# Optimization experiments

Hardware: AMD Instinct MI355X
Metric: run time of the kernel (lower is better)

The kernel has to match this reference:

```python
import jax, jax.numpy as jnp
import numpy as np

B, L, D = 8, 2048, 256
D_MODEL = 1024
NUM_SIGNALS = 16
MAX_POSITIONS = 4096
ROLE_OUTPUT = 2  # role id used for the CLS token


def setup_inputs() -> dict:
    key = jax.random.key(0)
    ks = jax.random.split(key, 12)
    emb = jax.random.normal(ks[0], (B, L, D), dtype=jnp.float32)
    pos = jax.random.randint(ks[1], (B, L), 1, MAX_POSITIONS + 1)          # pos >= 1 for real tokens
    sid = jax.random.randint(ks[2], (B, L), 0, NUM_SIGNALS)
    role = jax.random.randint(ks[3], (B, L), 0, 3)
    padding_mask = jax.random.uniform(ks[4], (B, L)) < 0.75                # True = real token
    # learned parameters
    proj_W = jax.random.normal(ks[5], (NUM_SIGNALS, D_MODEL, D), dtype=jnp.float32) * (1.0 / np.sqrt(D))
    proj_b = jax.random.normal(ks[6], (NUM_SIGNALS, D_MODEL), dtype=jnp.float32) * 0.01
    cls_content = jax.random.normal(ks[7], (D_MODEL,), dtype=jnp.float32)
    pos_embed = jax.random.normal(ks[8], (MAX_POSITIONS + 1, D_MODEL), dtype=jnp.float32)
    id_embed = jax.random.normal(ks[9], (NUM_SIGNALS + 1, D_MODEL), dtype=jnp.float32)
    role_embed = jax.random.normal(ks[10], (3, D_MODEL), dtype=jnp.float32)
    return dict(emb=emb, pos=pos, sid=sid, role=role, padding_mask=padding_mask,
                proj_W=proj_W, proj_b=proj_b, cls_content=cls_content,
                pos_embed=pos_embed, id_embed=id_embed, role_embed=role_embed)


def reference(emb, pos, sid, role, padding_mask,
              proj_W, proj_b, cls_content, pos_embed, id_embed, role_embed):
    Bv, Lv, _ = emb.shape
    S, d_model, _ = proj_W.shape
    cls_id = S

    # Grouped per-signal projection: one GEMM per signal id, select per token.
    tokens = jnp.zeros((Bv, Lv, d_model), dtype=emb.dtype)
    for s in range(S):
        proj_s = jnp.einsum('bld,ed->ble', emb, proj_W[s]) + proj_b[s]   # (B, L, d_model)
        keep = ((sid == s) & padding_mask)[..., None]
        tokens = jnp.where(keep, proj_s, tokens)

    # Prepend CLS
    cls = jnp.broadcast_to(cls_content[None, None, :], (Bv, 1, d_model))
    tokens = jnp.concatenate([cls, tokens], axis=1)                       # (B, L+1, d_model)

    pos_full = jnp.concatenate([jnp.zeros((Bv, 1), dtype=pos.dtype), pos], axis=1)
    sid_full = jnp.concatenate([jnp.full((Bv, 1), cls_id, dtype=sid.dtype), sid], axis=1)
    role_full = jnp.concatenate([jnp.full((Bv, 1), ROLE_OUTPUT, dtype=role.dtype), role], axis=1)

    tokens = tokens + pos_embed[pos_full] + id_embed[sid_full] + role_embed[role_full]

    attn_keep = jnp.concatenate([jnp.ones((Bv, 1), dtype=bool), padding_mask], axis=1)
    return tokens, attn_keep
```

## Files before the change

kernel.cpp:

```cpp
#include <hip/hip_runtime.h>
#include <hip/hip_bf16.h>
#include <stdint.h>

#define B_ 8
#define L_ 2048
#define NTOK 16384
#define DK 256
#define DM 1024
#define NS 16
#define LOUT 2049
#define TOK_OUT (B_*LOUT*DM)
#define ATTN_OUT (B_*LOUT)
#define PCAP 2048
#define UCAP 8192

typedef unsigned short u16;
typedef unsigned int u32;
typedef __bf16 bf16x8 __attribute__((ext_vector_type(8)));
typedef float f32x4 __attribute__((ext_vector_type(4)));

__device__ inline u32 packbf2(float lo, float hi) {
    u32 a, b;
    __builtin_memcpy(&a, &lo, 4);
    __builtin_memcpy(&b, &hi, 4);
    a = (a + 0x8000u) >> 16;
    b = (b + 0x8000u) & 0xFFFF0000u;
    return a | b;
}

__device__ inline void gll16(const void* g, void* l) {
    __builtin_amdgcn_global_load_lds(
        (const __attribute__((address_space(1))) unsigned int*)g,
        (__attribute__((address_space(3))) unsigned int*)l, 16, 0, 0);
}

#define WS_CUR 0
#define WS_UCUR 16
#define WS_WIDTH 32
#define WS_PERM 64
#define WS_UNM (64 + NS * PCAP)
#define EMB_OFF 262144ULL
#define W_OFF (EMB_OFF + 16384ULL * 512ULL)
#define WS_NEED (W_OFF + 16384ULL * 512ULL)

__device__ inline int sniff_width(const unsigned char* mb, int tid, int* sh) {
    if (tid == 0) { sh[0] = 0; sh[1] = 0; sh[2] = 0; }
    __syncthreads();
    int c1ge2 = 0, ge2 = 0, oddnz = 0;
    const u32* mw = (const u32*)mb;
    #pragma unroll
    for (int i = 0; i < 16; i++) {
        u32 x = mw[tid * 16 + i];
        u32 b0 = x & 0xFF, b1 = (x >> 8) & 0xFF, b2 = (x >> 16) & 0xFF, b3 = x >> 24;
        if (b1 >= 2) c1ge2 = 1;
        if (b0 >= 2 || b1 >= 2 || b2 >= 2 || b3 >= 2) ge2 = 1;
        if ((b1 | b3) != 0) oddnz = 1;
    }
    if (c1ge2) atomicOr(&sh[0], 1);
    if (ge2) atomicOr(&sh[1], 1);
    if (oddnz) atomicOr(&sh[2], 1);
    __syncthreads();
    if (sh[0]) return 2;
    if (sh[1]) return 4;
    if (sh[2]) return 1;
    return 4;
}

__device__ inline int decode_mask(const unsigned char* mb, int t, int width) {
    if (width == 1) return mb[t] != 0;
    if (width == 2) return ((const u16*)mb)[t] != 0;
    return ((const u32*)mb)[t] != 0;
}

#define SORT_B 64
#define PREP_GRID (SORT_B + 1024)

__global__ __launch_bounds__(256) void prep_all(
    const unsigned char* __restrict__ mb, const int* __restrict__ sid,
    const float* __restrict__ emb, const float* __restrict__ W,
    int* __restrict__ wsi, unsigned char* __restrict__ wsb) {
    __shared__ int sh[3];
    __shared__ int lcnt[NS], gbase[NS];
    __shared__ int lcnt_u, gbase_u;
    int bid = blockIdx.x;
    int tid = threadIdx.x;
    int lane = tid & 63;
    int wv = tid >> 6;

    if (bid < SORT_B) {
        if (tid < NS) lcnt[tid] = 0;
        if (tid == 0) lcnt_u = 0;
        int width = sniff_width(mb, tid, sh);
        if (bid == 0 && tid == 0) wsi[WS_WIDTH] = width;
        int t = bid * 256 + tid;
        int m = decode_mask(mb, t, width);
        int s = sid[t];
        int lr;
        if (m) lr = atomicAdd(&lcnt[s], 1);
        else   lr = atomicAdd(&lcnt_u, 1);
        __syncthreads();
        if (tid < NS) gbase[tid] = atomicAdd(&wsi[WS_CUR + tid], lcnt[tid]);
        if (tid == 0) gbase_u = atomicAdd(&wsi[WS_UCUR], lcnt_u);
        __syncthreads();
        if (m) {
            int r = gbase[s] + lr;
            if (r < PCAP) wsi[WS_PERM + s * PCAP + r] = t;
        } else {
            int r = gbase_u + lr;
            if (r < UCAP) wsi[WS_UNM + r] = t;
        }
        return;
    }

    int cb = bid - SORT_B;
    const float* src;
    u16* dst;
    if (cb < 512) {
        src = emb;
        dst = (u16*)(wsb + EMB_OFF);
    } else {
        cb -= 512;
        src = W;
        dst = (u16*)(wsb + W_OFF);
    }
    int r0 = cb * 32 + wv * 8;
    #pragma unroll 4
    for (int i = 0; i < 8; i++) {
        int r = r0 + i;
        float4 a = *(const float4*)(src + (size_t)r * DK + lane * 4);
        uint2 o;
        o.x = packbf2(a.x, a.y);
        o.y = packbf2(a.z, a.w);
        *(uint2*)(dst + (size_t)r * DK + lane * 4) = o;
    }
}

#define GG 1280
#define CLS_B0 (GG - 67)
#define ATTN_B0 (GG - 65)

__global__ __launch_bounds__(256, 4) void gemm_big(
    const unsigned char* __restrict__ mb,
    const int* __restrict__ pos, const int* __restrict__ sid,
    const int* __restrict__ role,
    const float* __restrict__ bias, const float* __restrict__ cls,
    const float* __restrict__ pos_emb, const float* __restrict__ id_emb,
    const float* __restrict__ role_emb,
    const int* __restrict__ wsi, const unsigned char* __restrict__ wsb,
    float* __restrict__ out) {
    __shared__ u16 As[2][128 * 32];
    __shared__ u16 Bs[2][128 * 32];
    __shared__ int toks[128];
    int bi = (int)blockIdx.x;
    int tid = threadIdx.x;
    int lane = tid & 63;
    int wv = tid >> 6;

    int cnts[NS];
    int mtot = 0;
    #pragma unroll
    for (int i = 0; i < NS; i++) {
        int c = wsi[WS_CUR + i];
        cnts[i] = c > PCAP ? PCAP : c;
        mtot += (cnts[i] + 127) >> 7;
    }
    int xcd = bi & 7;
    int j = bi >> 3;
    int m_lo = (xcd * mtot) >> 3;
    int m_hi = ((xcd + 1) * mtot) >> 3;
    int cm = m_hi - m_lo;
    bool doGemm = (cm > 0 && j < cm * 8);
    int s = -1, lrt = 0, n0 = 0;
    if (doGemm) {
        int nt = j / cm;
        int m = m_lo + (j - nt * cm);
        n0 = nt << 7;
        #pragma unroll
        for (int i = 0; i < NS; i++) {
            int rt = (cnts[i] + 127) >> 7;
            if (s < 0) {
                if (m < rt) { s = i; lrt = m; }
                else m -= rt;
            }
        }
        if (s < 0) doGemm = false;
    }

    if (doGemm) {
        int rowsValid = cnts[s] - lrt * 128;
        if (rowsValid > 128) rowsValid = 128;

        if (tid < 128) {
            int base = WS_PERM + s * PCAP + lrt * 128;
            toks[tid] = wsi[base + ((tid < rowsValid) ? tid : 0)];
        }
        __syncthreads();

        const u16* Eb = (const u16*)(wsb + EMB_OFF);
        const u16* Bb = (const u16*)(wsb + W_OFF) + (size_t)(s * DM + n0) * DK;

        int srow = lane >> 2;
        int slseg = lane & 3;
        int arow = wv * 16 + srow;
        int ags = (slseg - (arow >> 1)) & 3;
        const u16* AsrcLo = Eb + (size_t)toks[arow] * DK;
        const u16* AsrcHi = Eb + (size_t)toks[arow + 64] * DK;

        f32x4 acc[4][4];
        #pragma unroll
        for (int im = 0; im < 4; im++)
            #pragma unroll
            for (int jn = 0; jn < 4; jn++) acc[im][jn] = (f32x4){0.f, 0.f, 0.f, 0.f};

        int wm = wv & 1, wn = wv >> 1;
        int mcol = lane & 15;
        int quad = lane >> 4;

#define STAGE(kc, bf)                                                          \
        {                                                                      \
            gll16(AsrcLo + (kc) * 32 + ags * 8, &As[bf][(wv * 16) * 32]);      \
            gll16(AsrcHi + (kc) * 32 + ags * 8, &As[bf][(64 + wv * 16) * 32]); \
            gll16(Bb + (size_t)arow * DK + (kc) * 32 + ags * 8,                \
                  &Bs[bf][(wv * 16) * 32]);                                    \
            gll16(Bb + (size_t)(64 + arow) * DK + (kc) * 32 + ags * 8,         \
                  &Bs[bf][(64 + wv * 16) * 32]);                               \
        }

        STAGE(0, 0)
        #pragma unroll
        for (int kc = 0; kc < 8; ++kc) {
            __syncthreads();
            if (kc < 7) STAGE(kc + 1, (kc + 1) & 1)
            int bf = kc & 1;
            bf16x8 af[4], bfr[4];
            #pragma unroll
            for (int im = 0; im < 4; im++) {
                int row = wm * 64 + im * 16 + mcol;
                int sg = (quad + (row >> 1)) & 3;
                af[im] = *(const bf16x8*)(&As[bf][row * 32 + sg * 8]);
            }
            #pragma unroll
            for (int jn = 0; jn < 4; jn++) {
                int row = wn * 64 + jn * 16 + mcol;
                int sg = (quad + (row >> 1)) & 3;
                bfr[jn] = *(const bf16x8*)(&Bs[bf][row * 32 + sg * 8]);
            }
            #pragma unroll
            for (int im = 0; im < 4; im++)
                #pragma unroll
                for (int jn = 0; jn < 4; jn++)
                    acc[im][jn] = __builtin_amdgcn_mfma_f32_16x16x32_bf16(
                        af[im], bfr[jn], acc[im][jn], 0, 0, 0);
        }
#undef STAGE

        float bc[4];
        #pragma unroll
        for (int jn = 0; jn < 4; jn++) {
            int col = n0 + wn * 64 + jn * 16 + mcol;
            bc[jn] = bias[s * DM + col] + id_emb[s * DM + col];
        }
        #pragma unroll
        for (int im = 0; im < 4; im++) {
            #pragma unroll
            for (int r = 0; r < 4; r++) {
                int rowT = wm * 64 + im * 16 + quad * 4 + r;
                if (rowT >= rowsValid) continue;
                int t = toks[rowT];
                int p = pos[t];
                int ro = role[t];
                int b = t >> 11, l = t & 2047;
                size_t orow = (size_t)(b * LOUT + l + 1) * DM;
                const float* prow = pos_emb + (size_t)p * DM;
                const float* rrow = role_emb + (size_t)ro * DM;
                float pv[4], rv[4];
                #pragma unroll
                for (int jn = 0; jn < 4; jn++) {
                    int col = n0 + wn * 64 + jn * 16 + mcol;
                    pv[jn] = prow[col];
                    rv[jn] = rrow[col];
                }
                #pragma unroll
                for (int jn = 0; jn < 4; jn++) {
                    int col = n0 + wn * 64 + jn * 16 + mcol;
                    float val = acc[im][jn][r] + bc[jn] + pv[jn] + rv[jn];
                    __builtin_nontemporal_store(val, &out[orow + col]);
                }
            }
        }
    }

    {
        int ucnt = wsi[WS_UCUR];
        if (ucnt > UCAP) ucnt = UCAP;
        for (int idx = (GG - 1 - bi) * 4 + wv; idx < ucnt; idx += GG * 4) {
            int t = wsi[WS_UNM + idx];
            int p = pos[t], sd = sid[t], ro = role[t];
            int b = t >> 11, l = t & 2047;
            size_t orow = (size_t)(b * LOUT + l + 1) * DM;
            const float* pr = pos_emb + (size_t)p * DM;
            const float* ir = id_emb + (size_t)sd * DM;
            const float* rr = role_emb + (size_t)ro * DM;
            #pragma unroll
            for (int it = 0; it < 4; it++) {
                int c = it * 256 + lane * 4;
                f32x4 a = *(const f32x4*)(pr + c);
                f32x4 d = *(const f32x4*)(ir + c);
                f32x4 e = *(const f32x4*)(rr + c);
                f32x4 o = a + d + e;
                __builtin_nontemporal_store(o, (f32x4*)(out + orow + c));
            }
        }
        if (bi >= CLS_B0 && bi < ATTN_B0) {
            int b = (bi - CLS_B0) * 4 + wv;
            size_t orow = (size_t)(b * LOUT) * DM;
            #pragma unroll
            for (int it = 0; it < 4; it++) {
                int c = it * 256 + lane * 4;
                f32x4 cc = *(const f32x4*)(cls + c);
                f32x4 a = *(const f32x4*)(pos_emb + c);
                f32x4 d = *(const f32x4*)(id_emb + NS * DM + c);
                f32x4 e = *(const f32x4*)(role_emb + 2 * DM + c);
                f32x4 o = cc + a + d + e;
                *(f32x4*)(out + orow + c) = o;
            }
        }
        if (bi >= ATTN_B0) {
            int width = wsi[WS_WIDTH];
            int i = (bi - ATTN_B0) * 256 + tid;
            if (i < ATTN_OUT) {
                int b = i / LOUT;
                int jj = i - b * LOUT;
                float val = (jj == 0) ? 1.0f
                    : (float)decode_mask(mb, b * L_ + jj - 1, width);
                out[TOK_OUT + i] = val;
            }
        }
    }
}

extern "C" void kernel_launch(void* const* d_in, const int* in_sizes, int n_in,
                              void* d_out, int out_size, void* d_ws, size_t ws_size,
                              hipStream_t stream) {
    const float* emb = (const float*)d_in[0];
    const int* pos = (const int*)d_in[1];
    const int* sid = (const int*)d_in[2];
    const int* role = (const int*)d_in[3];
    const unsigned char* mask = (const unsigned char*)d_in[4];
    const float* W = (const float*)d_in[5];
    const float* bias = (const float*)d_in[6];
    const float* cls = (const float*)d_in[7];
    const float* pos_emb = (const float*)d_in[8];
    const float* id_emb = (const float*)d_in[9];
    const float* role_emb = (const float*)d_in[10];
    float* out = (float*)d_out;
    int* wsi = (int*)d_ws;
    unsigned char* wsb = (unsigned char*)d_ws;

    (void)hipMemsetAsync(wsi, 0, 64 * sizeof(int), stream);
    hipLaunchKernelGGL(prep_all, dim3(PREP_GRID), dim3(256), 0, stream,
                       mask, sid, emb, W, wsi, wsb);
    hipLaunchKernelGGL(gemm_big, dim3(GG), dim3(256), 0, stream,
                       mask, pos, sid, role, bias, cls, pos_emb, id_emb,
                       role_emb, wsi, wsb, out);
}
```

Measured before the change: 151.4 us.

## Fuse fp32-to-bf16 conversion into GEMM operand staging, drop prep pass

```diff
diff --git a/kernel.cpp b/kernel.cpp
--- a/kernel.cpp
+++ b/kernel.cpp
@@ -18,6 +18,7 @@
 typedef unsigned int u32;
 typedef __bf16 bf16x8 __attribute__((ext_vector_type(8)));
 typedef float f32x4 __attribute__((ext_vector_type(4)));
+typedef u32 u32x4 __attribute__((ext_vector_type(4)));
 
 __device__ inline u32 packbf2(float lo, float hi) {
     u32 a, b;
@@ -28,20 +29,11 @@
     return a | b;
 }
 
-__device__ inline void gll16(const void* g, void* l) {
-    __builtin_amdgcn_global_load_lds(
-        (const __attribute__((address_space(1))) unsigned int*)g,
-        (__attribute__((address_space(3))) unsigned int*)l, 16, 0, 0);
-}
-
 #define WS_CUR 0
 #define WS_UCUR 16
 #define WS_WIDTH 32
 #define WS_PERM 64
 #define WS_UNM (64 + NS * PCAP)
-#define EMB_OFF 262144ULL
-#define W_OFF (EMB_OFF + 16384ULL * 512ULL)
-#define WS_NEED (W_OFF + 16384ULL * 512ULL)
 
 __device__ inline int sniff_width(const unsigned char* mb, int tid, int* sh) {
     if (tid == 0) { sh[0] = 0; sh[1] = 0; sh[2] = 0; }
@@ -72,66 +64,35 @@
     return ((const u32*)mb)[t] != 0;
 }
 
-#define SORT_B 64
-#define PREP_GRID (SORT_B + 1024)
-
-__global__ __launch_bounds__(256) void prep_all(
+__global__ __launch_bounds__(256) void sort_kernel(
     const unsigned char* __restrict__ mb, const int* __restrict__ sid,
-    const float* __restrict__ emb, const float* __restrict__ W,
-    int* __restrict__ wsi, unsigned char* __restrict__ wsb) {
+    int* __restrict__ wsi) {
     __shared__ int sh[3];
     __shared__ int lcnt[NS], gbase[NS];
     __shared__ int lcnt_u, gbase_u;
     int bid = blockIdx.x;
     int tid = threadIdx.x;
-    int lane = tid & 63;
-    int wv = tid >> 6;
-
-    if (bid < SORT_B) {
-        if (tid < NS) lcnt[tid] = 0;
-        if (tid == 0) lcnt_u = 0;
-        int width = sniff_width(mb, tid, sh);
-        if (bid == 0 && tid == 0) wsi[WS_WIDTH] = width;
-        int t = bid * 256 + tid;
-        int m = decode_mask(mb, t, width);
-        int s = sid[t];
-        int lr;
-        if (m) lr = atomicAdd(&lcnt[s], 1);
-        else   lr = atomicAdd(&lcnt_u, 1);
-        __syncthreads();
-        if (tid < NS) gbase[tid] = atomicAdd(&wsi[WS_CUR + tid], lcnt[tid]);
-        if (tid == 0) gbase_u = atomicAdd(&wsi[WS_UCUR], lcnt_u);
-        __syncthreads();
-        if (m) {
-            int r = gbase[s] + lr;
-            if (r < PCAP) wsi[WS_PERM + s * PCAP + r] = t;
-        } else {
-            int r = gbase_u + lr;
-            if (r < UCAP) wsi[WS_UNM + r] = t;
-        }
-        return;
-    }
-
-    int cb = bid - SORT_B;
-    const float* src;
-    u16* dst;
-    if (cb < 512) {
-        src = emb;
-        dst = (u16*)(wsb + EMB_OFF);
+
+    if (tid < NS) lcnt[tid] = 0;
+    if (tid == 0) lcnt_u = 0;
+    int width = sniff_width(mb, tid, sh);
+    if (bid == 0 && tid == 0) wsi[WS_WIDTH] = width;
+    int t = bid * 256 + tid;
+    int m = decode_mask(mb, t, width);
+    int s = sid[t];
+    int lr;
+    if (m) lr = atomicAdd(&lcnt[s], 1);
+    else   lr = atomicAdd(&lcnt_u, 1);
+    __syncthreads();
+    if (tid < NS) gbase[tid] = atomicAdd(&wsi[WS_CUR + tid], lcnt[tid]);
+    if (tid == 0) gbase_u = atomicAdd(&wsi[WS_UCUR], lcnt_u);
+    __syncthreads();
+    if (m) {
+        int r = gbase[s] + lr;
+        if (r < PCAP) wsi[WS_PERM + s * PCAP + r] = t;
     } else {
-        cb -= 512;
-        src = W;
-        dst = (u16*)(wsb + W_OFF);
-    }
-    int r0 = cb * 32 + wv * 8;
-    #pragma unroll 4
-    for (int i = 0; i < 8; i++) {
-        int r = r0 + i;
-        float4 a = *(const float4*)(src + (size_t)r * DK + lane * 4);
-        uint2 o;
-        o.x = packbf2(a.x, a.y);
-        o.y = packbf2(a.z, a.w);
-        *(uint2*)(dst + (size_t)r * DK + lane * 4) = o;
+        int r = gbase_u + lr;
+        if (r < UCAP) wsi[WS_UNM + r] = t;
     }
 }
 
@@ -143,11 +104,11 @@
     const unsigned char* __restrict__ mb,
     const int* __restrict__ pos, const int* __restrict__ sid,
     const int* __restrict__ role,
+    const float* __restrict__ emb, const float* __restrict__ W,
     const float* __restrict__ bias, const float* __restrict__ cls,
     const float* __restrict__ pos_emb, const float* __restrict__ id_emb,
     const float* __restrict__ role_emb,
-    const int* __restrict__ wsi, const unsigned char* __restrict__ wsb,
-    float* __restrict__ out) {
+    const int* __restrict__ wsi, float* __restrict__ out) {
     __shared__ u16 As[2][128 * 32];
     __shared__ u16 Bs[2][128 * 32];
     __shared__ int toks[128];
@@ -196,15 +157,42 @@
         }
         __syncthreads();
 
-        const u16* Eb = (const u16*)(wsb + EMB_OFF);
-        const u16* Bb = (const u16*)(wsb + W_OFF) + (size_t)(s * DM + n0) * DK;
-
-        int srow = lane >> 2;
-        int slseg = lane & 3;
-        int arow = wv * 16 + srow;
-        int ags = (slseg - (arow >> 1)) & 3;
-        const u16* AsrcLo = Eb + (size_t)toks[arow] * DK;
-        const u16* AsrcHi = Eb + (size_t)toks[arow + 64] * DK;
+        int srow = tid >> 1;
+        int spair = tid & 1;
+        int ga0 = spair * 2;
+        int ga1 = ga0 + 1;
+        int sl0 = (ga0 + (srow >> 1)) & 3;
+        int sl1 = (ga1 + (srow >> 1)) & 3;
+        const float* Ag = emb + (size_t)toks[srow] * DK;
+        const float* Bg = W + ((size_t)s * DM + n0 + srow) * DK;
+
+        f32x4 la[4], lb[4];
+#define LOADS(kc)                                                              \
+        {                                                                      \
+            la[0] = *(const f32x4*)(Ag + (kc) * 32 + ga0 * 8);                 \
+            la[1] = *(const f32x4*)(Ag + (kc) * 32 + ga0 * 8 + 4);             \
+            la[2] = *(const f32x4*)(Ag + (kc) * 32 + ga1 * 8);                 \
+            la[3] = *(const f32x4*)(Ag + (kc) * 32 + ga1 * 8 + 4);             \
+            lb[0] = *(const f32x4*)(Bg + (kc) * 32 + ga0 * 8);                 \
+            lb[1] = *(const f32x4*)(Bg + (kc) * 32 + ga0 * 8 + 4);             \
+            lb[2] = *(const f32x4*)(Bg + (kc) * 32 + ga1 * 8);                 \
+            lb[3] = *(const f32x4*)(Bg + (kc) * 32 + ga1 * 8 + 4);             \
+        }
+#define WRITES(bf)                                                             \
+        {                                                                      \
+            u32x4 wa0 = {packbf2(la[0].x, la[0].y), packbf2(la[0].z, la[0].w), \
+                         packbf2(la[1].x, la[1].y), packbf2(la[1].z, la[1].w)};\
+            u32x4 wa1 = {packbf2(la[2].x, la[2].y), packbf2(la[2].z, la[2].w), \
+                         packbf2(la[3].x, la[3].y), packbf2(la[3].z, la[3].w)};\
+            u32x4 wb0 = {packbf2(lb[0].x, lb[0].y), packbf2(lb[0].z, lb[0].w), \
+                         packbf2(lb[1].x, lb[1].y), packbf2(lb[1].z, lb[1].w)};\
+            u32x4 wb1 = {packbf2(lb[2].x, lb[2].y), packbf2(lb[2].z, lb[2].w), \
+                         packbf2(lb[3].x, lb[3].y), packbf2(lb[3].z, lb[3].w)};\
+            *(u32x4*)&As[bf][srow * 32 + sl0 * 8] = wa0;                       \
+            *(u32x4*)&As[bf][srow * 32 + sl1 * 8] = wa1;                       \
+            *(u32x4*)&Bs[bf][srow * 32 + sl0 * 8] = wb0;                       \
+            *(u32x4*)&Bs[bf][srow * 32 + sl1 * 8] = wb1;                       \
+        }
 
         f32x4 acc[4][4];
         #pragma unroll
@@ -216,21 +204,12 @@
         int mcol = lane & 15;
         int quad = lane >> 4;
 
-#define STAGE(kc, bf)                                                          \
-        {                                                                      \
-            gll16(AsrcLo + (kc) * 32 + ags * 8, &As[bf][(wv * 16) * 32]);      \
-            gll16(AsrcHi + (kc) * 32 + ags * 8, &As[bf][(64 + wv * 16) * 32]); \
-            gll16(Bb + (size_t)arow * DK + (kc) * 32 + ags * 8,                \
-                  &Bs[bf][(wv * 16) * 32]);                                    \
-            gll16(Bb + (size_t)(64 + arow) * DK + (kc) * 32 + ags * 8,         \
-                  &Bs[bf][(64 + wv * 16) * 32]);                               \
-        }
-
-        STAGE(0, 0)
+        LOADS(0)
+        WRITES(0)
+        __syncthreads();
         #pragma unroll
         for (int kc = 0; kc < 8; ++kc) {
-            __syncthreads();
-            if (kc < 7) STAGE(kc + 1, (kc + 1) & 1)
+            if (kc < 7) LOADS(kc + 1)
             int bf = kc & 1;
             bf16x8 af[4], bfr[4];
             #pragma unroll
@@ -251,8 +230,14 @@
                 for (int jn = 0; jn < 4; jn++)
                     acc[im][jn] = __builtin_amdgcn_mfma_f32_16x16x32_bf16(
                         af[im], bfr[jn], acc[im][jn], 0, 0, 0);
-        }
-#undef STAGE
+            if (kc < 7) {
+                __syncthreads();
+                WRITES(bf ^ 1)
+                __syncthreads();
+            }
+        }
+#undef LOADS
+#undef WRITES
 
         float bc[4];
         #pragma unroll
@@ -355,12 +340,11 @@
     const float* role_emb = (const float*)d_in[10];
     float* out = (float*)d_out;
     int* wsi = (int*)d_ws;
-    unsigned char* wsb = (unsigned char*)d_ws;
 
     (void)hipMemsetAsync(wsi, 0, 64 * sizeof(int), stream);
-    hipLaunchKernelGGL(prep_all, dim3(PREP_GRID), dim3(256), 0, stream,
-                       mask, sid, emb, W, wsi, wsb);
+    hipLaunchKernelGGL(sort_kernel, dim3(64), dim3(256), 0, stream,
+                       mask, sid, wsi);
     hipLaunchKernelGGL(gemm_big, dim3(GG), dim3(256), 0, stream,
-                       mask, pos, sid, role, bias, cls, pos_emb, id_emb,
-                       role_emb, wsi, wsb, out);
-}
+                       mask, pos, sid, role, emb, W, bias, cls, pos_emb,
+                       id_emb, role_emb, wsi, out);
+}
```

After: 164.9 us. +8.9%, slower.
